# Optimization experiments

Measured on AMD Instinct MI355X. Metric: run time of the kernel, lower is better.

Reference implementation:

```python
import jax, jax.numpy as jnp
import numpy as np

EPS = 1e-6

def setup_inputs() -> dict:
    key = jax.random.key(0)
    k1, k2 = jax.random.split(key)
    S, B, H, F = 2048, 4, 2048, 8192
    x = jax.random.normal(k1, (S, B, H), dtype=jnp.float32)
    scale = jnp.ones((H,), dtype=jnp.float32)
    ln_bias = jnp.zeros((H,), dtype=jnp.float32)
    kernel = jax.random.normal(k2, (H, F), dtype=jnp.float32) * 0.02  # ~variance_scaling fan_in
    return {"x": x, "scale": scale, "ln_bias": ln_bias, "kernel": kernel}

def reference(x, scale, ln_bias, kernel):
    # LayerNorm over last (hidden) axis, stats in fp32
    mu = jnp.mean(x, axis=-1, keepdims=True)
    var = jnp.mean(jnp.square(x - mu), axis=-1, keepdims=True)
    y = (x - mu) * jax.lax.rsqrt(var + EPS) * scale + ln_bias  # [S,B,H]
    # Dense: contract hidden axis against kernel [H,F]
    z = jnp.einsum('sbh,hf->sbf', y, kernel)  # [S,B,F]
    # return_layernorm_output=True -> (dense_out, ln_out)
    return (z, y)
```

## Files before the change

### kernel.cpp

```cpp
#include <hip/hip_runtime.h>
#include <stdint.h>


typedef __attribute__((ext_vector_type(8))) short short8;
typedef __attribute__((ext_vector_type(4))) float floatx4;

__device__ __forceinline__ unsigned short f2bf(float f) {
    unsigned u = __builtin_bit_cast(unsigned, f);
    u += 0x7fffu + ((u >> 16) & 1u);
    return (unsigned short)(u >> 16);
}

__global__ __launch_bounds__(256) void ln_kernel(
    const float* __restrict__ x, const float* __restrict__ scale,
    const float* __restrict__ bias, float* __restrict__ y,
    unsigned short* __restrict__ ybf, int H)
{
    const int row = blockIdx.x;
    const float* xr = x + (size_t)row * H;
    const int tid = threadIdx.x;

    float4 v0 = ((const float4*)xr)[tid];
    float4 v1 = ((const float4*)xr)[tid + 256];

    float s  = v0.x + v0.y + v0.z + v0.w + v1.x + v1.y + v1.z + v1.w;
    float ss = v0.x*v0.x + v0.y*v0.y + v0.z*v0.z + v0.w*v0.w
             + v1.x*v1.x + v1.y*v1.y + v1.z*v1.z + v1.w*v1.w;

    #pragma unroll
    for (int off = 32; off > 0; off >>= 1) {
        s  += __shfl_down(s,  off, 64);
        ss += __shfl_down(ss, off, 64);
    }
    __shared__ float rs[4], rq[4];
    if ((tid & 63) == 0) { rs[tid >> 6] = s; rq[tid >> 6] = ss; }
    __syncthreads();
    float ts = rs[0] + rs[1] + rs[2] + rs[3];
    float tq = rq[0] + rq[1] + rq[2] + rq[3];
    float mean = ts / (float)H;
    float var  = tq / (float)H - mean * mean;
    float rstd = rsqrtf(var + 1e-6f);

    float4 sc0 = ((const float4*)scale)[tid];
    float4 sc1 = ((const float4*)scale)[tid + 256];
    float4 b0  = ((const float4*)bias)[tid];
    float4 b1  = ((const float4*)bias)[tid + 256];

    float4 o0, o1;
    o0.x = (v0.x - mean) * rstd * sc0.x + b0.x;
    o0.y = (v0.y - mean) * rstd * sc0.y + b0.y;
    o0.z = (v0.z - mean) * rstd * sc0.z + b0.z;
    o0.w = (v0.w - mean) * rstd * sc0.w + b0.w;
    o1.x = (v1.x - mean) * rstd * sc1.x + b1.x;
    o1.y = (v1.y - mean) * rstd * sc1.y + b1.y;
    o1.z = (v1.z - mean) * rstd * sc1.z + b1.z;
    o1.w = (v1.w - mean) * rstd * sc1.w + b1.w;

    float* yr = y + (size_t)row * H;
    ((float4*)yr)[tid]       = o0;
    ((float4*)yr)[tid + 256] = o1;

    unsigned short* br = ybf + (size_t)row * H;
    uint2 p0, p1;
    p0.x = (unsigned)f2bf(o0.x) | ((unsigned)f2bf(o0.y) << 16);
    p0.y = (unsigned)f2bf(o0.z) | ((unsigned)f2bf(o0.w) << 16);
    p1.x = (unsigned)f2bf(o1.x) | ((unsigned)f2bf(o1.y) << 16);
    p1.y = (unsigned)f2bf(o1.z) | ((unsigned)f2bf(o1.w) << 16);
    ((uint2*)br)[tid]       = p0;
    ((uint2*)br)[tid + 256] = p1;
}

__global__ __launch_bounds__(256) void transpose_cast_kernel(
    const float* __restrict__ W, unsigned short* __restrict__ Bt,
    int K, int F)
{
    __shared__ float tile[64][65];
    const int kBase = blockIdx.y * 64;
    const int fBase = blockIdx.x * 64;
    const int tid = threadIdx.x;

    #pragma unroll
    for (int p = 0; p < 4; ++p) {
        int kl = (tid >> 4) + p * 16;
        int fl = (tid & 15) * 4;
        float4 v = *(const float4*)&W[(size_t)(kBase + kl) * F + fBase + fl];
        tile[kl][fl]     = v.x;
        tile[kl][fl + 1] = v.y;
        tile[kl][fl + 2] = v.z;
        tile[kl][fl + 3] = v.w;
    }
    __syncthreads();

    #pragma unroll
    for (int p = 0; p < 2; ++p) {
        int fl = (tid >> 3) + p * 32;
        int k8 = (tid & 7) * 8;
        unsigned w[4];
        #pragma unroll
        for (int j = 0; j < 4; ++j) {
            unsigned lo = f2bf(tile[k8 + 2*j][fl]);
            unsigned hi = f2bf(tile[k8 + 2*j + 1][fl]);
            w[j] = lo | (hi << 16);
        }
        uint4 out = make_uint4(w[0], w[1], w[2], w[3]);
        *(uint4*)&Bt[(size_t)(fBase + fl) * K + kBase + k8] = out;
    }
}

#define GBM 256
#define GBN 256
#define GBK 32

__device__ __forceinline__ void gload16(const unsigned short* src,
                                        unsigned short* dst) {
    __builtin_amdgcn_global_load_lds(
        (const __attribute__((address_space(1))) unsigned int*)src,
        (__attribute__((address_space(3))) unsigned int*)dst, 16, 0, 0);
}

__device__ __forceinline__ void stage_op(
    const unsigned short* __restrict__ g, unsigned short* dst,
    int t, int K, int tid)
{
    #pragma unroll
    for (int i = 0; i < 2; ++i) {
        int e = i * 512 + tid;
        int r = e >> 2;
        int c = (e & 3) ^ ((r >> 1) & 3);
        gload16(g + (size_t)r * K + t * GBK + c * 8, dst + e * 8);
    }
}

__global__ __launch_bounds__(512, 2) void gemm_bf16_8w(
    const unsigned short* __restrict__ A,
    const unsigned short* __restrict__ Bt,
    float* __restrict__ C,
    int M, int N, int K)
{
    __shared__ __align__(128) unsigned short lds[4][16384];

    const int tid   = threadIdx.x;
    const int lane  = tid & 63;
    const int wave  = tid >> 6;
    const int waveM = wave >> 2;
    const int waveN = wave & 3;
    const int quad  = lane >> 4;
    const int l16   = lane & 15;
    const int soff  = (quad ^ ((l16 >> 1) & 3)) * 8;
    const int rowA0 = waveM * 128 + l16;
    const int rowB0 = waveN * 64 + l16;

    const int nwg = gridDim.x;
    const int cpx = nwg >> 3;
    const int bid = blockIdx.x;
    const int wg  = (bid & 7) * cpx + (bid >> 3);
    const int tilesN = N >> 8;
    const int tm = wg / tilesN;
    const int tn = wg % tilesN;

    const unsigned short* gA = A  + (size_t)tm * GBM * K;
    const unsigned short* gB = Bt + (size_t)tn * GBN * K;

    const int NT = K >> 5;

    floatx4 acc[8][4] = {};

    stage_op(gA, &lds[0][0],    0, K, tid);
    stage_op(gB, &lds[0][8192], 0, K, tid);
    stage_op(gA, &lds[1][0],    1, K, tid);
    stage_op(gB, &lds[1][8192], 1, K, tid);
    stage_op(gA, &lds[2][0],    2, K, tid);
    stage_op(gB, &lds[2][8192], 2, K, tid);
    asm volatile("s_waitcnt vmcnt(8)" ::: "memory");
    __builtin_amdgcn_s_barrier();

    for (int t = 0; t < NT; t += 4) {
        #pragma unroll
        for (int u = 0; u < 4; ++u) {
            const int tt = t + u;
            const unsigned short* bufA = &lds[u][0];
            const unsigned short* bufB = &lds[u][8192];
            unsigned short* pre = &lds[(u + 3) & 3][0];
            int ts = tt + 3; if (ts > NT - 1) ts = NT - 1;

            stage_op(gA, pre, ts, K, tid);
            stage_op(gB, pre + 8192, ts, K, tid);

            short8 a0[4], a1[4], b[4];
            #pragma unroll
            for (int i = 0; i < 4; ++i)
                a0[i] = *(const short8*)(bufA + (rowA0 + i * 16) * 32 + soff);
            #pragma unroll
            for (int j = 0; j < 4; ++j)
                b[j] = *(const short8*)(bufB + (rowB0 + j * 16) * 32 + soff);
            #pragma unroll
            for (int i = 0; i < 4; ++i)
                a1[i] = *(const short8*)(bufA + (rowA0 + 64 + i * 16) * 32 + soff);

            __builtin_amdgcn_s_setprio(1);
            #pragma unroll
            for (int i = 0; i < 4; ++i)
                #pragma unroll
                for (int j = 0; j < 4; ++j)
                    acc[i][j] = __builtin_amdgcn_mfma_f32_16x16x32_bf16(
                        a0[i], b[j], acc[i][j], 0, 0, 0);
            #pragma unroll
            for (int i = 0; i < 4; ++i)
                #pragma unroll
                for (int j = 0; j < 4; ++j)
                    acc[4 + i][j] = __builtin_amdgcn_mfma_f32_16x16x32_bf16(
                        a1[i], b[j], acc[4 + i][j], 0, 0, 0);
            __builtin_amdgcn_s_setprio(0);

            asm volatile("s_waitcnt vmcnt(8) lgkmcnt(0)" ::: "memory");
            __builtin_amdgcn_s_barrier();
        }
    }

    const size_t bm = (size_t)tm * GBM;
    const size_t bn = (size_t)tn * GBN;
    #pragma unroll
    for (int mi = 0; mi < 8; ++mi) {
        #pragma unroll
        for (int ni = 0; ni < 4; ++ni) {
            size_t col = bn + (size_t)waveN * 64 + ni * 16 + l16;
            #pragma unroll
            for (int r = 0; r < 4; ++r) {
                size_t row = bm + (size_t)waveM * 128 + mi * 16 + quad * 4 + r;
                C[row * N + col] = acc[mi][ni][r];
            }
        }
    }
}

extern "C" void kernel_launch(void* const* d_in, const int* in_sizes, int n_in,
                              void* d_out, int out_size, void* d_ws, size_t ws_size,
                              hipStream_t stream) {
    const float* x      = (const float*)d_in[0];
    const float* scale  = (const float*)d_in[1];
    const float* lnbias = (const float*)d_in[2];
    const float* W      = (const float*)d_in[3];

    const int H = in_sizes[1];
    const int M = in_sizes[0] / H;
    const int F = in_sizes[3] / H;

    float* z = (float*)d_out;
    float* y = z + (size_t)M * F;

    unsigned short* Abf = (unsigned short*)d_ws;
    unsigned short* Btb = Abf + (size_t)M * H;

    ln_kernel<<<M, 256, 0, stream>>>(x, scale, lnbias, y, Abf, H);
    transpose_cast_kernel<<<dim3(F / 64, H / 64), 256, 0, stream>>>(W, Btb, H, F);
    gemm_bf16_8w<<<dim3((M / GBM) * (F / GBN)), 512, 0, stream>>>(Abf, Btb, z, M, F, H);
}
```

Measured before the change: 682.1 us.

## Software-pipeline LDS fragment reads one stage ahead of MFMA in GEMM loop

Restructures the GEMM main loop so each step reads the next tile's LDS fragments into one register set while running MFMAs on the previous tile's fragments held in another set, alternating between the two. This is meant to hide LDS read latency behind matrix-core work, which the old loop exposed by reading fragments and then issuing MFMAs in sequence. The cost is an extra 12 short8 registers per thread, which at launch bounds (512,2) could cause spills. It also changes the ring-buffer prefetch indexing, so the barrier and wait-count placement must still protect buffers that are being overwritten.

```diff
diff --git a/kernel.cpp b/kernel.cpp
--- a/kernel.cpp
+++ b/kernel.cpp
@@ -129,6 +129,42 @@
         int c = (e & 3) ^ ((r >> 1) & 3);
         gload16(g + (size_t)r * K + t * GBK + c * 8, dst + e * 8);
     }
+}
+
+__device__ __forceinline__ void read_frags(
+    const unsigned short* bufA, const unsigned short* bufB,
+    int rowA0, int rowB0, int soff,
+    short8 (&a0)[4], short8 (&a1)[4], short8 (&b)[4])
+{
+    #pragma unroll
+    for (int i = 0; i < 4; ++i)
+        a0[i] = *(const short8*)(bufA + (rowA0 + i * 16) * 32 + soff);
+    #pragma unroll
+    for (int j = 0; j < 4; ++j)
+        b[j] = *(const short8*)(bufB + (rowB0 + j * 16) * 32 + soff);
+    #pragma unroll
+    for (int i = 0; i < 4; ++i)
+        a1[i] = *(const short8*)(bufA + (rowA0 + 64 + i * 16) * 32 + soff);
+}
+
+__device__ __forceinline__ void mfma_tile(
+    const short8 (&a0)[4], const short8 (&a1)[4], const short8 (&b)[4],
+    floatx4 (&acc)[8][4])
+{
+    __builtin_amdgcn_s_setprio(1);
+    #pragma unroll
+    for (int i = 0; i < 4; ++i)
+        #pragma unroll
+        for (int j = 0; j < 4; ++j)
+            acc[i][j] = __builtin_amdgcn_mfma_f32_16x16x32_bf16(
+                a0[i], b[j], acc[i][j], 0, 0, 0);
+    #pragma unroll
+    for (int i = 0; i < 4; ++i)
+        #pragma unroll
+        for (int j = 0; j < 4; ++j)
+            acc[4 + i][j] = __builtin_amdgcn_mfma_f32_16x16x32_bf16(
+                a1[i], b[j], acc[4 + i][j], 0, 0, 0);
+    __builtin_amdgcn_s_setprio(0);
 }
 
 __global__ __launch_bounds__(512, 2) void gemm_bf16_8w(
@@ -164,6 +200,8 @@
     const int NT = K >> 5;
 
     floatx4 acc[8][4] = {};
+    short8 xa0[4], xa1[4], xb[4];
+    short8 ya0[4], ya1[4], yb[4];
 
     stage_op(gA, &lds[0][0],    0, K, tid);
     stage_op(gB, &lds[0][8192], 0, K, tid);
@@ -174,48 +212,45 @@
     asm volatile("s_waitcnt vmcnt(8)" ::: "memory");
     __builtin_amdgcn_s_barrier();
 
-    for (int t = 0; t < NT; t += 4) {
-        #pragma unroll
-        for (int u = 0; u < 4; ++u) {
-            const int tt = t + u;
-            const unsigned short* bufA = &lds[u][0];
-            const unsigned short* bufB = &lds[u][8192];
-            unsigned short* pre = &lds[(u + 3) & 3][0];
-            int ts = tt + 3; if (ts > NT - 1) ts = NT - 1;
-
-            stage_op(gA, pre, ts, K, tid);
-            stage_op(gB, pre + 8192, ts, K, tid);
-
-            short8 a0[4], a1[4], b[4];
-            #pragma unroll
-            for (int i = 0; i < 4; ++i)
-                a0[i] = *(const short8*)(bufA + (rowA0 + i * 16) * 32 + soff);
-            #pragma unroll
-            for (int j = 0; j < 4; ++j)
-                b[j] = *(const short8*)(bufB + (rowB0 + j * 16) * 32 + soff);
-            #pragma unroll
-            for (int i = 0; i < 4; ++i)
-                a1[i] = *(const short8*)(bufA + (rowA0 + 64 + i * 16) * 32 + soff);
-
-            __builtin_amdgcn_s_setprio(1);
-            #pragma unroll
-            for (int i = 0; i < 4; ++i)
-                #pragma unroll
-                for (int j = 0; j < 4; ++j)
-                    acc[i][j] = __builtin_amdgcn_mfma_f32_16x16x32_bf16(
-                        a0[i], b[j], acc[i][j], 0, 0, 0);
-            #pragma unroll
-            for (int i = 0; i < 4; ++i)
-                #pragma unroll
-                for (int j = 0; j < 4; ++j)
-                    acc[4 + i][j] = __builtin_amdgcn_mfma_f32_16x16x32_bf16(
-                        a1[i], b[j], acc[4 + i][j], 0, 0, 0);
-            __builtin_amdgcn_s_setprio(0);
-
-            asm volatile("s_waitcnt vmcnt(8) lgkmcnt(0)" ::: "memory");
-            __builtin_amdgcn_s_barrier();
-        }
-    }
+    for (unsigned t = 0; t < (unsigned)NT; t += 4) {
+        {
+            int ts = (int)t + 3; if (ts > NT - 1) ts = NT - 1;
+            stage_op(gA, &lds[3][0],    ts, K, tid);
+            stage_op(gB, &lds[3][8192], ts, K, tid);
+            read_frags(&lds[0][0], &lds[0][8192], rowA0, rowB0, soff, xa0, xa1, xb);
+            if (t > 0) mfma_tile(ya0, ya1, yb, acc);
+            asm volatile("s_waitcnt vmcnt(8) lgkmcnt(0)" ::: "memory");
+            __builtin_amdgcn_s_barrier();
+        }
+        {
+            int ts = (int)t + 4; if (ts > NT - 1) ts = NT - 1;
+            stage_op(gA, &lds[0][0],    ts, K, tid);
+            stage_op(gB, &lds[0][8192], ts, K, tid);
+            read_frags(&lds[1][0], &lds[1][8192], rowA0, rowB0, soff, ya0, ya1, yb);
+            mfma_tile(xa0, xa1, xb, acc);
+            asm volatile("s_waitcnt vmcnt(8) lgkmcnt(0)" ::: "memory");
+            __builtin_amdgcn_s_barrier();
+        }
+        {
+            int ts = (int)t + 5; if (ts > NT - 1) ts = NT - 1;
+            stage_op(gA, &lds[1][0],    ts, K, tid);
+            stage_op(gB, &lds[1][8192], ts, K, tid);
+            read_frags(&lds[2][0], &lds[2][8192], rowA0, rowB0, soff, xa0, xa1, xb);
+            mfma_tile(ya0, ya1, yb, acc);
+            asm volatile("s_waitcnt vmcnt(8) lgkmcnt(0)" ::: "memory");
+            __builtin_amdgcn_s_barrier();
+        }
+        {
+            int ts = (int)t + 6; if (ts > NT - 1) ts = NT - 1;
+            stage_op(gA, &lds[2][0],    ts, K, tid);
+            stage_op(gB, &lds[2][8192], ts, K, tid);
+            read_frags(&lds[3][0], &lds[3][8192], rowA0, rowB0, soff, ya0, ya1, yb);
+            mfma_tile(xa0, xa1, xb, acc);
+            asm volatile("s_waitcnt vmcnt(8) lgkmcnt(0)" ::: "memory");
+            __builtin_amdgcn_s_barrier();
+        }
+    }
+    mfma_tile(ya0, ya1, yb, acc);
 
     const size_t bm = (size_t)tm * GBM;
     const size_t bn = (size_t)tn * GBN;
```

After: 685.3 us. No clear change (+0.5%).
